# Performance work log

Hardware: AMD Instinct MI355X
Metric: run time of the kernel (lower is better)

Reference implementation:

```python
import jax, jax.numpy as jnp
import numpy as np

B, L, D, NL, VOCAB = 2, 8192, 512, 8, 32
FFT_LEN = 2 * L  # causal linear conv via zero-padded FFT


def layernorm(x, g, b, eps=1e-5):
    mu = jnp.mean(x, axis=-1, keepdims=True)
    var = jnp.var(x, axis=-1, keepdims=True)
    return (x - mu) * jax.lax.rsqrt(var + eps) * g + b


def fftconv(v, h, bias):
    # v: [B, d, L], h: [d, L] long implicit filter, bias: [d] skip (the Hyena 'D' term)
    vf = jnp.fft.rfft(v, n=FFT_LEN)
    hf = jnp.fft.rfft(h, n=FFT_LEN)
    y = jnp.fft.irfft(vf * hf[None], n=FFT_LEN)[..., :L]
    return y + v * bias[:, None]


def short_conv(p, w, b):
    # causal depthwise conv, kernel size 3: p [B, C, L], w [C, 3], b [C]
    pp = jnp.pad(p, ((0, 0), (0, 0), (2, 0)))
    out = jax.lax.conv_general_dilated(pp, w[:, None, :], (1,), 'VALID',
                                       feature_group_count=p.shape[1])
    return out + b[None, :, None]


def setup_inputs() -> dict:
    key = jax.random.key(0)
    ks = jax.random.split(key, 12)
    rn = lambda k, sh, s: jax.random.normal(k, sh, jnp.float32) * s
    d = D
    return {
        'input_ids': jax.random.randint(ks[0], (B, L), 0, VOCAB),
        'emb': rn(ks[1], (VOCAB, d), 0.02),
        'ln1_g': jnp.ones((NL, d)), 'ln1_b': jnp.zeros((NL, d)),
        'Win': rn(ks[2], (NL, d, 3 * d), d ** -0.5), 'bin_': jnp.zeros((NL, 3 * d)),
        'convw': rn(ks[3], (NL, 3 * d, 3), 3 ** -0.5), 'convb': jnp.zeros((NL, 3 * d)),
        'h': rn(ks[4], (NL, d, L), L ** -0.5),  # implicit long filter, materialized
        'Db': rn(ks[5], (NL, d), 1.0),
        'Wout': rn(ks[6], (NL, d, d), d ** -0.5), 'bout': jnp.zeros((NL, d)),
        'ln2_g': jnp.ones((NL, d)), 'ln2_b': jnp.zeros((NL, d)),
        'W1': rn(ks[7], (NL, d, 4 * d), d ** -0.5), 'b1': jnp.zeros((NL, 4 * d)),
        'W2': rn(ks[8], (NL, 4 * d, d), (4 * d) ** -0.5), 'b2': jnp.zeros((NL, d)),
        'lnf_g': jnp.ones((d,)), 'lnf_b': jnp.zeros((d,)),
    }


def reference(input_ids, emb, ln1_g, ln1_b, Win, bin_, convw, convb, h, Db,
              Wout, bout, ln2_g, ln2_b, W1, b1, W2, b2, lnf_g, lnf_b):
    u = emb[input_ids]  # [B, L, d]
    for l in range(NL):  # structural loop over layers
        z = layernorm(u, ln1_g[l], ln1_b[l])
        p = (jnp.einsum('bld,de->ble', z, Win[l]) + bin_[l]).transpose(0, 2, 1)  # [B,3d,L]
        p = short_conv(p, convw[l], convb[l])
        x2, x1, v = jnp.split(p, 3, axis=1)  # each [B, d, L]
        v = fftconv(v * x1, h[l], Db[l])     # gate then FFT long conv (order-2 Hyena)
        y = (v * x2).transpose(0, 2, 1)      # output gate -> [B, L, d]
        u = u + jnp.einsum('bld,de->ble', y, Wout[l]) + bout[l]
        z = layernorm(u, ln2_g[l], ln2_b[l])
        hmid = jax.nn.gelu(jnp.einsum('bld,df->blf', z, W1[l]) + b1[l])
        u = u + jnp.einsum('blf,fd->bld', hmid, W2[l]) + b2[l]
    return layernorm(u, lnf_g, lnf_b)  # last_hidden_state [B, L, d]
```

## Files before the change

### kernel.cpp

```cpp
#include <hip/hip_runtime.h>
#include <hip/hip_bf16.h>
#include <math.h>

#define BB 2
#define LL 8192
#define DD 512
#define NLAYER 8
#define TD 1536
#define HD 2048
#define NFFT 16384
#define BLD (BB*LL*DD)
#define BLH ((size_t)BB*LL*HD)

typedef unsigned short u16;
typedef unsigned int   u32;
typedef __bf16 bf16x8 __attribute__((ext_vector_type(8)));
typedef float  f32x4  __attribute__((ext_vector_type(4)));

__device__ __forceinline__ u16 f2bf(float f) {
    union { float f; u32 u; } v; v.f = f;
    u32 r = v.u + 0x7FFF + ((v.u >> 16) & 1);
    return (u16)(r >> 16);
}
__device__ __forceinline__ float bf2f(u16 h) {
    union { u32 u; float f; } v; v.u = (u32)h << 16; return v.f;
}

__device__ __forceinline__ void async_g2l_16(const u16* g, u16* l) {
    __builtin_amdgcn_global_load_lds(
        (const __attribute__((address_space(1))) void*)g,
        (__attribute__((address_space(3))) void*)l,
        16, 0, 0);
}

__device__ __forceinline__ float2 cmul(float2 a, float2 b) {
    return make_float2(a.x * b.x - a.y * b.y, a.x * b.y + a.y * b.x);
}
__device__ __forceinline__ float2 cmulc(float2 a, float2 b) {
    return make_float2(a.x * b.x + a.y * b.y, a.y * b.x - a.x * b.y);
}
__device__ __forceinline__ float2 cadd(float2 a, float2 b) {
    return make_float2(a.x + b.x, a.y + b.y);
}
__device__ __forceinline__ float2 csub(float2 a, float2 b) {
    return make_float2(a.x - b.x, a.y - b.y);
}
__device__ __forceinline__ int drev14(int x) {
    return ((x & 3) << 12) | (((x >> 2) & 3) << 10) | (((x >> 4) & 3) << 8) |
           (((x >> 6) & 3) << 6) | (((x >> 8) & 3) << 4) | (((x >> 10) & 3) << 2) |
           ((x >> 12) & 3);
}

__global__ void twiddle_kernel(float* twf) {
    int k = blockIdx.x * 256 + threadIdx.x;
    if (k < NFFT) {
        double ang = -2.0 * M_PI * (double)k / (double)NFFT;
        twf[2 * k]     = (float)cos(ang);
        twf[2 * k + 1] = (float)sin(ang);
    }
}

__global__ void embed_kernel(const int* __restrict__ ids,
                             const float* __restrict__ emb,
                             float* __restrict__ u) {
    int i = blockIdx.x * 256 + threadIdx.x;
    if (i < BLD) {
        int row = i >> 9;
        int d   = i & (DD - 1);
        u[i] = emb[ids[row] * DD + d];
    }
}

__global__ __launch_bounds__(256)
void wprep_kernel(const float* __restrict__ W, u16* __restrict__ WtH,
                  u16* __restrict__ WtL, int K, int N, long srcStride, long dstStride) {
    __shared__ float t[64][65];
    const float* src = W + (size_t)blockIdx.z * srcStride;
    u16* dsth = WtH + (size_t)blockIdx.z * dstStride;
    u16* dstl = WtL + (size_t)blockIdx.z * dstStride;
    int n0 = blockIdx.x * 64, k0 = blockIdx.y * 64;
    int tc = threadIdx.x & 63, tr = threadIdx.x >> 6;
    for (int r = tr; r < 64; r += 4)
        t[r][tc] = src[(size_t)(k0 + r) * N + n0 + tc];
    __syncthreads();
    for (int r = tr; r < 64; r += 4) {
        float v = t[tc][r];
        u16 h = f2bf(v);
        dsth[(size_t)(n0 + r) * K + k0 + tc] = h;
        dstl[(size_t)(n0 + r) * K + k0 + tc] = f2bf(v - bf2f(h));
    }
}

template<int MODE>
__global__ __launch_bounds__(128)
void ln_kernel(const float* __restrict__ x, void* __restrict__ out,
               void* __restrict__ outL,
               const float* __restrict__ g, const float* __restrict__ b) {
    int row = blockIdx.x;
    const float4* xr = (const float4*)(x + (size_t)row * DD);
    int t = threadIdx.x;
    float4 v = xr[t];
    float s  = v.x + v.y + v.z + v.w;
    float ss = v.x * v.x + v.y * v.y + v.z * v.z + v.w * v.w;
    for (int off = 32; off; off >>= 1) {
        s  += __shfl_down(s, off);
        ss += __shfl_down(ss, off);
    }
    __shared__ float sm[4];
    if ((t & 63) == 0) { sm[(t >> 6) * 2] = s; sm[(t >> 6) * 2 + 1] = ss; }
    __syncthreads();
    float S = sm[0] + sm[2], SS = sm[1] + sm[3];
    float mu  = S * (1.0f / DD);
    float var = SS * (1.0f / DD) - mu * mu;
    float rs  = rsqrtf(var + 1e-5f);
    float4 gg = ((const float4*)g)[t];
    float4 bb = ((const float4*)b)[t];
    float o[4];
    o[0] = (v.x - mu) * rs * gg.x + bb.x;
    o[1] = (v.y - mu) * rs * gg.y + bb.y;
    o[2] = (v.z - mu) * rs * gg.z + bb.z;
    o[3] = (v.w - mu) * rs * gg.w + bb.w;
    if (MODE == 1) {
        u16 h[4], lo[4];
#pragma unroll
        for (int i = 0; i < 4; i++) {
            h[i]  = f2bf(o[i]);
            lo[i] = f2bf(o[i] - bf2f(h[i]));
        }
        uint2 ph, pl;
        ph.x = (u32)h[0] | ((u32)h[1] << 16);  ph.y = (u32)h[2] | ((u32)h[3] << 16);
        pl.x = (u32)lo[0] | ((u32)lo[1] << 16); pl.y = (u32)lo[2] | ((u32)lo[3] << 16);
        ((uint2*)((u16*)out  + (size_t)row * DD))[t] = ph;
        ((uint2*)((u16*)outL + (size_t)row * DD))[t] = pl;
    } else {
        float4 of = {o[0], o[1], o[2], o[3]};
        ((float4*)((float*)out + (size_t)row * DD))[t] = of;
    }
}

__device__ __forceinline__ float gelu_f(float x) {
    float x3 = x * x * x;
    float t  = tanhf(0.79788456080286541f * (x + 0.044715f * x3));
    return 0.5f * x * (1.0f + t);
}

template<int OUT, bool GELU, int PASSES>
__global__ __launch_bounds__(256)
void mfma_gemm3(const u16* __restrict__ Ah, const u16* __restrict__ Al,
                const u16* __restrict__ Bh, const u16* __restrict__ Bl,
                const float* __restrict__ bias,
                float* __restrict__ Cf, u16* __restrict__ Ch, u16* __restrict__ Cl,
                int M, int N, int K) {
    __shared__ u16 AsH[128 * 32];
    __shared__ u16 AsL[128 * 32];
    __shared__ u16 BsH[128 * 32];
    __shared__ u16 BsL[(PASSES == 3) ? 128 * 32 : 8];
    int m0 = blockIdx.y * 128, n0 = blockIdx.x * 128;
    int tid = threadIdx.x;
    int w = tid >> 6, l = tid & 63;
    int wr = w >> 1, wc = w & 1;

    int ch0 = w * 2, ch1 = ch0 + 1;
    size_t offA0 = (size_t)(m0 + ch0 * 16 + (l >> 2)) * K + (l & 3) * 8;
    size_t offA1 = (size_t)(m0 + ch1 * 16 + (l >> 2)) * K + (l & 3) * 8;
    size_t offB0 = (size_t)(n0 + ch0 * 16 + (l >> 2)) * K + (l & 3) * 8;
    size_t offB1 = (size_t)(n0 + ch1 * 16 + (l >> 2)) * K + (l & 3) * 8;

    f32x4 acc[4][4] = {};
    int arow = wr * 64 + (l & 15);
    int brow = wc * 64 + (l & 15);
    int kc   = (l >> 4) * 8;

    for (int k0 = 0; k0 < K; k0 += 32) {
        async_g2l_16(Ah + offA0 + k0, &AsH[ch0 * 512]);
        async_g2l_16(Ah + offA1 + k0, &AsH[ch1 * 512]);
        async_g2l_16(Al + offA0 + k0, &AsL[ch0 * 512]);
        async_g2l_16(Al + offA1 + k0, &AsL[ch1 * 512]);
        async_g2l_16(Bh + offB0 + k0, &BsH[ch0 * 512]);
        async_g2l_16(Bh + offB1 + k0, &BsH[ch1 * 512]);
        if (PASSES == 3) {
            async_g2l_16(Bl + offB0 + k0, &BsL[ch0 * 512]);
            async_g2l_16(Bl + offB1 + k0, &BsL[ch1 * 512]);
        }
        __syncthreads();
        bf16x8 ah[4], al[4], bh[4], bl[4];
#pragma unroll
        for (int i = 0; i < 4; i++) {
            ah[i] = *(const bf16x8*)&AsH[(arow + i * 16) * 32 + kc];
            al[i] = *(const bf16x8*)&AsL[(arow + i * 16) * 32 + kc];
            bh[i] = *(const bf16x8*)&BsH[(brow + i * 16) * 32 + kc];
            if (PASSES == 3)
                bl[i] = *(const bf16x8*)&BsL[(brow + i * 16) * 32 + kc];
        }
#pragma unroll
        for (int mi = 0; mi < 4; mi++)
#pragma unroll
            for (int ni = 0; ni < 4; ni++) {
                acc[mi][ni] = __builtin_amdgcn_mfma_f32_16x16x32_bf16(
                    ah[mi], bh[ni], acc[mi][ni], 0, 0, 0);
                acc[mi][ni] = __builtin_amdgcn_mfma_f32_16x16x32_bf16(
                    al[mi], bh[ni], acc[mi][ni], 0, 0, 0);
                if (PASSES == 3)
                    acc[mi][ni] = __builtin_amdgcn_mfma_f32_16x16x32_bf16(
                        ah[mi], bl[ni], acc[mi][ni], 0, 0, 0);
            }
        __syncthreads();
    }

    int lr = l >> 4, lc = l & 15;
#pragma unroll
    for (int mi = 0; mi < 4; mi++) {
#pragma unroll
        for (int ni = 0; ni < 4; ni++) {
            int col = n0 + wc * 64 + ni * 16 + lc;
            float bv = bias[col];
            int rowb = m0 + wr * 64 + mi * 16 + lr * 4;
#pragma unroll
            for (int r = 0; r < 4; r++) {
                float v = acc[mi][ni][r] + bv;
                if (GELU) v = gelu_f(v);
                size_t off = (size_t)(rowb + r) * N + col;
                if (OUT == 0) {
                    Cf[off] = v;
                } else if (OUT == 1) {
                    u16 h = f2bf(v);
                    Ch[off] = h;
                    Cl[off] = f2bf(v - bf2f(h));
                } else {
                    Cf[off] += v;
                }
            }
        }
    }
}

__global__ __launch_bounds__(256)
void conv_gate_kernel(const float* __restrict__ p, const float* __restrict__ cw,
                      const float* __restrict__ cb, float* __restrict__ vg,
                      float* __restrict__ x2s) {
    __shared__ float tvg[64][65];
    __shared__ float tx2[64][65];
    int b = blockIdx.z, c0 = blockIdx.y * 64, l0 = blockIdx.x * 64;
    int tc = threadIdx.x & 63, tr = threadIdx.x >> 6;
    const float* pb = p + (size_t)b * LL * TD;
    int cx2 = c0 + tc;
    int cx1 = DD + c0 + tc;
    int cv  = 2 * DD + c0 + tc;
    float w20 = cw[cx2 * 3], w21 = cw[cx2 * 3 + 1], w22 = cw[cx2 * 3 + 2], bx2 = cb[cx2];
    float w10 = cw[cx1 * 3], w11 = cw[cx1 * 3 + 1], w12 = cw[cx1 * 3 + 2], bx1 = cb[cx1];
    float wv0 = cw[cv * 3],  wv1 = cw[cv * 3 + 1],  wv2 = cw[cv * 3 + 2],  bv  = cb[cv];
    for (int r = tr; r < 64; r += 4) {
        int l = l0 + r;
        size_t o0 = (size_t)l * TD;
        float p2a = (l >= 2) ? pb[o0 - 2 * TD + cx2] : 0.f;
        float p1a = (l >= 1) ? pb[o0 - TD + cx2] : 0.f;
        float p0a = pb[o0 + cx2];
        float p2b = (l >= 2) ? pb[o0 - 2 * TD + cx1] : 0.f;
        float p1b = (l >= 1) ? pb[o0 - TD + cx1] : 0.f;
        float p0b = pb[o0 + cx1];
        float p2c = (l >= 2) ? pb[o0 - 2 * TD + cv] : 0.f;
        float p1c = (l >= 1) ? pb[o0 - TD + cv] : 0.f;
        float p0c = pb[o0 + cv];
        float x2v = w20 * p2a + w21 * p1a + w22 * p0a + bx2;
        float x1v = w10 * p2b + w11 * p1b + w12 * p0b + bx1;
        float vv  = wv0 * p2c + wv1 * p1c + wv2 * p0c + bv;
        tx2[r][tc] = x2v;
        tvg[r][tc] = vv * x1v;
    }
    __syncthreads();
    for (int r = tr; r < 64; r += 4) {
        size_t o = ((size_t)b * DD + c0 + r) * LL + l0 + tc;
        vg[o]  = tvg[tc][r];
        x2s[o] = tx2[tc][r];
    }
}

__global__ __launch_bounds__(256)
void ytr_kernel(const float* __restrict__ yg, u16* __restrict__ yh,
                u16* __restrict__ yl) {
    __shared__ float t[64][65];
    int b = blockIdx.z, c0 = blockIdx.y * 64, l0 = blockIdx.x * 64;
    int tc = threadIdx.x & 63, tr = threadIdx.x >> 6;
    for (int r = tr; r < 64; r += 4)
        t[r][tc] = yg[((size_t)b * DD + c0 + r) * LL + l0 + tc];
    __syncthreads();
    for (int r = tr; r < 64; r += 4) {
        float v = t[tc][r];
        u16 h = f2bf(v);
        size_t o = ((size_t)(b * LL + l0 + r)) * DD + c0 + tc;
        yh[o] = h;
        yl[o] = f2bf(v - bf2f(h));
    }
}

__device__ __forceinline__ void fft4_fwd(float2* ld, const float2* __restrict__ tw, int tid) {
    for (int s = 0; s < 7; s++) {
        int lm = 14 - 2 * s, lq = lm - 2;
        int Q = 1 << lq;
        __syncthreads();
        for (int g = tid; g < NFFT / 4; g += 1024) {
            int j = g & (Q - 1);
            int base = ((g >> lq) << lm) + j;
            float2 x0 = ld[base], x1 = ld[base + Q], x2 = ld[base + 2 * Q], x3 = ld[base + 3 * Q];
            float2 a = cadd(x0, x2), b = csub(x0, x2);
            float2 c = cadd(x1, x3), d = csub(x1, x3);
            float2 mid = make_float2(d.y, -d.x);
            float2 u0 = cadd(a, c);
            float2 u1 = cadd(b, mid);
            float2 u2 = csub(a, c);
            float2 u3 = csub(b, mid);
            int e = j << (2 * s);
            if (e) {
                u1 = cmul(u1, tw[e]);
                u2 = cmul(u2, tw[2 * e]);
                u3 = cmul(u3, tw[3 * e]);
            }
            ld[base] = u0; ld[base + Q] = u1; ld[base + 2 * Q] = u2; ld[base + 3 * Q] = u3;
        }
    }
    __syncthreads();
}

__device__ __forceinline__ void fft4_inv(float2* ld, const float2* __restrict__ tw, int tid) {
    for (int s = 6; s >= 0; s--) {
        int lm = 14 - 2 * s, lq = lm - 2;
        int Q = 1 << lq;
        __syncthreads();
        for (int g = tid; g < NFFT / 4; g += 1024) {
            int j = g & (Q - 1);
            int base = ((g >> lq) << lm) + j;
            int e = j << (2 * s);
            float2 v0 = ld[base];
            float2 v1 = ld[base + Q], v2 = ld[base + 2 * Q], v3 = ld[base + 3 * Q];
            if (e) {
                v1 = cmulc(v1, tw[e]);
                v2 = cmulc(v2, tw[2 * e]);
                v3 = cmulc(v3, tw[3 * e]);
            }
            float2 a = cadd(v0, v2), b = csub(v0, v2);
            float2 c = cadd(v1, v3), d = csub(v1, v3);
            float2 id = make_float2(-d.y, d.x);
            ld[base]         = cadd(a, c);
            ld[base + Q]     = cadd(b, id);
            ld[base + 2 * Q] = csub(a, c);
            ld[base + 3 * Q] = csub(b, id);
        }
    }
    __syncthreads();
}


__global__ __launch_bounds__(1024)
void hf_kernel(const float* __restrict__ h, float2* __restrict__ Hf1,
               float2* __restrict__ Hf2, const float* __restrict__ twf) {
    __shared__ float2 ld[NFFT];
    int cp = blockIdx.x;
    const float* h1 = h + (size_t)(2 * cp) * LL;
    const float* h2 = h + (size_t)(2 * cp + 1) * LL;
    const float2* tw = (const float2*)twf;
    int tid = threadIdx.x;
    for (int i = tid; i < LL; i += 1024) ld[i] = make_float2(h1[i], h2[i]);
    for (int i = LL + tid; i < NFFT; i += 1024) ld[i] = make_float2(0.f, 0.f);
    fft4_fwd(ld, tw, tid);
    float2* o1 = Hf1 + (size_t)cp * NFFT;
    float2* o2 = Hf2 + (size_t)cp * NFFT;
    for (int i = tid; i < NFFT / 2; i += 1024) {
        int p  = ((i >> 1) << 2) | (i & 1);
        int k  = drev14(p);
        int kc = (NFFT - k) & (NFFT - 1);
        int pc = drev14(kc);
        float2 Zk = ld[p], Zc = ld[pc];
        float2 F1 = make_float2(0.5f * (Zk.x + Zc.x), 0.5f * (Zk.y - Zc.y));
        float2 F2 = make_float2(0.5f * (Zk.y + Zc.y), 0.5f * (Zc.x - Zk.x));
        o1[p]  = F1;
        o2[p]  = F2;
        o1[pc] = make_float2(F1.x, -F1.y);
        o2[pc] = make_float2(F2.x, -F2.y);
    }
    if (tid == 0) {
        float2 Zk = ld[2];
        o1[2] = make_float2(Zk.x, 0.f);
        o2[2] = make_float2(Zk.y, 0.f);
    }
}

__global__ __launch_bounds__(1024)
void fftconv_kernel(const float* __restrict__ vg, const float* __restrict__ x2s,
                    const float2* __restrict__ Hf1, const float2* __restrict__ Hf2,
                    const float* __restrict__ Db, const float* __restrict__ twf,
                    float* __restrict__ yg) {
    __shared__ float2 ld[NFFT];
    int bcp = blockIdx.x;
    int b = bcp >> 8, cp = bcp & 255;
    int c1 = 2 * cp, c2 = 2 * cp + 1;
    const float* v1 = vg + ((size_t)b * DD + c1) * LL;
    const float* v2 = vg + ((size_t)b * DD + c2) * LL;
    const float2* tw = (const float2*)twf;
    int tid = threadIdx.x;
    for (int i = tid; i < LL; i += 1024) ld[i] = make_float2(v1[i], v2[i]);
    for (int i = LL + tid; i < NFFT; i += 1024) ld[i] = make_float2(0.f, 0.f);
    fft4_fwd(ld, tw, tid);
    const float2* H1 = Hf1 + (size_t)cp * NFFT;
    const float2* H2 = Hf2 + (size_t)cp * NFFT;
    for (int i = tid; i < NFFT / 2; i += 1024) {
        int p  = ((i >> 1) << 2) | (i & 1);
        int k  = drev14(p);
        int kc = (NFFT - k) & (NFFT - 1);
        int pc = drev14(kc);
        float2 Zk = ld[p], Zc = ld[pc];
        float2 F1 = make_float2(0.5f * (Zk.x + Zc.x), 0.5f * (Zk.y - Zc.y));
        float2 F2 = make_float2(0.5f * (Zk.y + Zc.y), 0.5f * (Zc.x - Zk.x));
        float2 c1v = cmul(F1, H1[p]);
        float2 c2v = cmul(F2, H2[p]);
        ld[p]  = make_float2(c1v.x - c2v.y, c1v.y + c2v.x);
        ld[pc] = make_float2(c1v.x + c2v.y, c2v.x - c1v.y);
    }
    if (tid == 0) {
        float2 Zk = ld[2];
        float2 c1v = cmul(make_float2(Zk.x, 0.f), H1[2]);
        float2 c2v = cmul(make_float2(Zk.y, 0.f), H2[2]);
        ld[2] = make_float2(c1v.x - c2v.y, c1v.y + c2v.x);
    }
    fft4_inv(ld, tw, tid);
    float db1 = Db[c1], db2 = Db[c2];
    const float* x21 = x2s + ((size_t)b * DD + c1) * LL;
    const float* x22 = x2s + ((size_t)b * DD + c2) * LL;
    float* o1 = yg + ((size_t)b * DD + c1) * LL;
    float* o2 = yg + ((size_t)b * DD + c2) * LL;
    for (int i = tid; i < LL; i += 1024) {
        float y1 = ld[i].x * (1.0f / NFFT) + v1[i] * db1;
        float y2 = ld[i].y * (1.0f / NFFT) + v2[i] * db2;
        o1[i] = y1 * x21[i];
        o2[i] = y2 * x22[i];
    }
}

extern "C" void kernel_launch(void* const* d_in, const int* in_sizes, int n_in,
                              void* d_out, int out_size, void* d_ws, size_t ws_size,
                              hipStream_t stream) {
    const int*   ids   = (const int*)  d_in[0];
    const float* emb   = (const float*)d_in[1];
    const float* ln1_g = (const float*)d_in[2];
    const float* ln1_b = (const float*)d_in[3];
    const float* Win   = (const float*)d_in[4];
    const float* bin_  = (const float*)d_in[5];
    const float* convw = (const float*)d_in[6];
    const float* convb = (const float*)d_in[7];
    const float* hflt  = (const float*)d_in[8];
    const float* Db    = (const float*)d_in[9];
    const float* Wout  = (const float*)d_in[10];
    const float* bout  = (const float*)d_in[11];
    const float* ln2_g = (const float*)d_in[12];
    const float* ln2_b = (const float*)d_in[13];
    const float* W1    = (const float*)d_in[14];
    const float* b1    = (const float*)d_in[15];
    const float* W2    = (const float*)d_in[16];
    const float* b2    = (const float*)d_in[17];
    const float* lnf_g = (const float*)d_in[18];
    const float* lnf_b = (const float*)d_in[19];

    char* p_ = (char*)d_ws;
    auto alloc = [&](size_t bytes) {
        char* r = p_; p_ += (bytes + 255) & ~(size_t)255; return r;
    };
    float* u   = (float*)alloc((size_t)BLD * 4);
    u16* zh    = (u16*)  alloc((size_t)BLD * 2);
    u16* zl    = (u16*)  alloc((size_t)BLD * 2);
    char* uni  = alloc(2 * BLH * 2);
    float* pf  = (float*)uni;
    float* yg  = (float*)uni;
    u16* hmh   = (u16*)uni;
    u16* hml   = hmh + BLH;
    float* vg  = (float*)alloc((size_t)BLD * 4);
    float* x2s = (float*)alloc((size_t)BLD * 4);
    u16* yh    = (u16*)  alloc((size_t)BLD * 2);
    u16* yl    = (u16*)  alloc((size_t)BLD * 2);
    float2* Hf1 = (float2*)alloc((size_t)(DD / 2) * NFFT * 8);
    float2* Hf2 = (float2*)alloc((size_t)(DD / 2) * NFFT * 8);
    float* tw  = (float*)alloc((size_t)2 * NFFT * 4);
    u16* WtInH = (u16*)alloc((size_t)NLAYER * TD * DD * 2);
    u16* WtInL = (u16*)alloc((size_t)NLAYER * TD * DD * 2);
    u16* WtOutH= (u16*)alloc((size_t)NLAYER * DD * DD * 2);
    u16* WtOutL= (u16*)alloc((size_t)NLAYER * DD * DD * 2);
    u16* Wt1H  = (u16*)alloc((size_t)NLAYER * DD * HD * 2);
    u16* Wt1L  = (u16*)alloc((size_t)NLAYER * DD * HD * 2);
    u16* Wt2H  = (u16*)alloc((size_t)NLAYER * HD * DD * 2);
    u16* Wt2L  = (u16*)alloc((size_t)NLAYER * HD * DD * 2);

    twiddle_kernel<<<(NFFT + 255) / 256, 256, 0, stream>>>(tw);
    embed_kernel<<<(BLD + 255) / 256, 256, 0, stream>>>(ids, emb, u);
    wprep_kernel<<<dim3(TD / 64, DD / 64, NLAYER), 256, 0, stream>>>(
        Win, WtInH, WtInL, DD, TD, (long)DD * TD, (long)TD * DD);
    wprep_kernel<<<dim3(DD / 64, DD / 64, NLAYER), 256, 0, stream>>>(
        Wout, WtOutH, WtOutL, DD, DD, (long)DD * DD, (long)DD * DD);
    wprep_kernel<<<dim3(HD / 64, DD / 64, NLAYER), 256, 0, stream>>>(
        W1, Wt1H, Wt1L, DD, HD, (long)DD * HD, (long)DD * HD);
    wprep_kernel<<<dim3(DD / 64, HD / 64, NLAYER), 256, 0, stream>>>(
        W2, Wt2H, Wt2L, HD, DD, (long)HD * DD, (long)HD * DD);

    for (int l = 0; l < NLAYER; l++) {
        ln_kernel<1><<<BB * LL, 128, 0, stream>>>(u, zh, zl,
            ln1_g + l * DD, ln1_b + l * DD);

        mfma_gemm3<0, false, 3><<<dim3(TD / 128, (BB * LL) / 128), 256, 0, stream>>>(
            zh, zl, WtInH + (size_t)l * TD * DD, WtInL + (size_t)l * TD * DD,
            bin_ + (size_t)l * TD, pf, nullptr, nullptr, BB * LL, TD, DD);

        conv_gate_kernel<<<dim3(LL / 64, DD / 64, BB), 256, 0, stream>>>(
            pf, convw + (size_t)l * TD * 3, convb + (size_t)l * TD, vg, x2s);

        hf_kernel<<<DD / 2, 1024, 0, stream>>>(hflt + (size_t)l * DD * LL, Hf1, Hf2, tw);

        fftconv_kernel<<<BB * (DD / 2), 1024, 0, stream>>>(
            vg, x2s, Hf1, Hf2, Db + (size_t)l * DD, tw, yg);

        ytr_kernel<<<dim3(LL / 64, DD / 64, BB), 256, 0, stream>>>(yg, yh, yl);

        mfma_gemm3<2, false, 3><<<dim3(DD / 128, (BB * LL) / 128), 256, 0, stream>>>(
            yh, yl, WtOutH + (size_t)l * DD * DD, WtOutL + (size_t)l * DD * DD,
            bout + (size_t)l * DD, u, nullptr, nullptr, BB * LL, DD, DD);

        ln_kernel<1><<<BB * LL, 128, 0, stream>>>(u, zh, zl,
            ln2_g + l * DD, ln2_b + l * DD);

        mfma_gemm3<1, true, 2><<<dim3(HD / 128, (BB * LL) / 128), 256, 0, stream>>>(
            zh, zl, Wt1H + (size_t)l * DD * HD, Wt1L + (size_t)l * DD * HD,
            b1 + (size_t)l * HD, nullptr, hmh, hml, BB * LL, HD, DD);

        mfma_gemm3<2, false, 2><<<dim3(DD / 128, (BB * LL) / 128), 256, 0, stream>>>(
            hmh, hml, Wt2H + (size_t)l * HD * DD, Wt2L + (size_t)l * HD * DD,
            b2 + (size_t)l * DD, u, nullptr, nullptr, BB * LL, DD, HD);
    }

    ln_kernel<0><<<BB * LL, 128, 0, stream>>>(u, (float*)d_out, nullptr, lnf_g, lnf_b);
}
```

Before: 5.501 ms.

## Replace paired-channel 16K complex FFT with per-channel 8K half-length real FFT

```diff
diff --git a/kernel.cpp b/kernel.cpp
--- a/kernel.cpp
+++ b/kernel.cpp
@@ -9,6 +9,7 @@
 #define TD 1536
 #define HD 2048
 #define NFFT 16384
+#define NHALF 8192
 #define BLD (BB*LL*DD)
 #define BLH ((size_t)BB*LL*HD)
 
@@ -45,10 +46,12 @@
 __device__ __forceinline__ float2 csub(float2 a, float2 b) {
     return make_float2(a.x - b.x, a.y - b.y);
 }
-__device__ __forceinline__ int drev14(int x) {
-    return ((x & 3) << 12) | (((x >> 2) & 3) << 10) | (((x >> 4) & 3) << 8) |
-           (((x >> 6) & 3) << 6) | (((x >> 8) & 3) << 4) | (((x >> 10) & 3) << 2) |
-           ((x >> 12) & 3);
+__device__ __forceinline__ int drev12(int m) {
+    return ((m & 3) << 10) | (((m >> 2) & 3) << 8) | (((m >> 4) & 3) << 6) |
+           (((m >> 6) & 3) << 4) | (((m >> 8) & 3) << 2) | ((m >> 10) & 3);
+}
+__device__ __forceinline__ int perm8k(int k) {
+    return ((k & 1) << 12) + drev12(k >> 1);
 }
 
 __global__ void twiddle_kernel(float* twf) {
@@ -293,14 +296,22 @@
     }
 }
 
-__device__ __forceinline__ void fft4_fwd(float2* ld, const float2* __restrict__ tw, int tid) {
-    for (int s = 0; s < 7; s++) {
-        int lm = 14 - 2 * s, lq = lm - 2;
+__device__ __forceinline__ void fft8192_fwd(float2* ld, const float2* __restrict__ tw, int tid) {
+    __syncthreads();
+    for (int n = tid; n < 4096; n += 1024) {
+        float2 a = ld[n], b = ld[n + 4096];
+        ld[n] = cadd(a, b);
+        float2 d = csub(a, b);
+        ld[n + 4096] = n ? cmul(d, tw[2 * n]) : d;
+    }
+    for (int s = 0; s < 6; s++) {
+        int lm = 12 - 2 * s, lq = lm - 2;
         int Q = 1 << lq;
         __syncthreads();
-        for (int g = tid; g < NFFT / 4; g += 1024) {
-            int j = g & (Q - 1);
-            int base = ((g >> lq) << lm) + j;
+        for (int g = tid; g < 2048; g += 1024) {
+            int half = g >> 10, gg = g & 1023;
+            int j = gg & (Q - 1);
+            int base = (half << 12) + ((gg >> lq) << lm) + j;
             float2 x0 = ld[base], x1 = ld[base + Q], x2 = ld[base + 2 * Q], x3 = ld[base + 3 * Q];
             float2 a = cadd(x0, x2), b = csub(x0, x2);
             float2 c = cadd(x1, x3), d = csub(x1, x3);
@@ -311,9 +322,9 @@
             float2 u3 = csub(b, mid);
             int e = j << (2 * s);
             if (e) {
-                u1 = cmul(u1, tw[e]);
-                u2 = cmul(u2, tw[2 * e]);
-                u3 = cmul(u3, tw[3 * e]);
+                u1 = cmul(u1, tw[4 * e]);
+                u2 = cmul(u2, tw[8 * e]);
+                u3 = cmul(u3, tw[12 * e]);
             }
             ld[base] = u0; ld[base + Q] = u1; ld[base + 2 * Q] = u2; ld[base + 3 * Q] = u3;
         }
@@ -321,21 +332,22 @@
     __syncthreads();
 }
 
-__device__ __forceinline__ void fft4_inv(float2* ld, const float2* __restrict__ tw, int tid) {
-    for (int s = 6; s >= 0; s--) {
-        int lm = 14 - 2 * s, lq = lm - 2;
+__device__ __forceinline__ void fft8192_inv(float2* ld, const float2* __restrict__ tw, int tid) {
+    for (int s = 5; s >= 0; s--) {
+        int lm = 12 - 2 * s, lq = lm - 2;
         int Q = 1 << lq;
         __syncthreads();
-        for (int g = tid; g < NFFT / 4; g += 1024) {
-            int j = g & (Q - 1);
-            int base = ((g >> lq) << lm) + j;
+        for (int g = tid; g < 2048; g += 1024) {
+            int half = g >> 10, gg = g & 1023;
+            int j = gg & (Q - 1);
+            int base = (half << 12) + ((gg >> lq) << lm) + j;
             int e = j << (2 * s);
             float2 v0 = ld[base];
             float2 v1 = ld[base + Q], v2 = ld[base + 2 * Q], v3 = ld[base + 3 * Q];
             if (e) {
-                v1 = cmulc(v1, tw[e]);
-                v2 = cmulc(v2, tw[2 * e]);
-                v3 = cmulc(v3, tw[3 * e]);
+                v1 = cmulc(v1, tw[4 * e]);
+                v2 = cmulc(v2, tw[8 * e]);
+                v3 = cmulc(v3, tw[12 * e]);
             }
             float2 a = cadd(v0, v2), b = csub(v0, v2);
             float2 c = cadd(v1, v3), d = csub(v1, v3);
@@ -347,91 +359,101 @@
         }
     }
     __syncthreads();
-}
-
-
-__global__ __launch_bounds__(1024)
-void hf_kernel(const float* __restrict__ h, float2* __restrict__ Hf1,
-               float2* __restrict__ Hf2, const float* __restrict__ twf) {
-    __shared__ float2 ld[NFFT];
-    int cp = blockIdx.x;
-    const float* h1 = h + (size_t)(2 * cp) * LL;
-    const float* h2 = h + (size_t)(2 * cp + 1) * LL;
+    for (int n = tid; n < 4096; n += 1024) {
+        float2 a = ld[n];
+        float2 b = ld[n + 4096];
+        if (n) b = cmulc(b, tw[2 * n]);
+        ld[n] = cadd(a, b);
+        ld[n + 4096] = csub(a, b);
+    }
+    __syncthreads();
+}
+
+__global__ __launch_bounds__(1024, 8)
+void hf_kernel(const float* __restrict__ h, float2* __restrict__ HfA,
+               float2* __restrict__ HfB, const float* __restrict__ twf) {
+    __shared__ float2 ld[NHALF];
+    int c = blockIdx.x;
+    const float2* hp = (const float2*)(h + (size_t)c * LL);
     const float2* tw = (const float2*)twf;
     int tid = threadIdx.x;
-    for (int i = tid; i < LL; i += 1024) ld[i] = make_float2(h1[i], h2[i]);
-    for (int i = LL + tid; i < NFFT; i += 1024) ld[i] = make_float2(0.f, 0.f);
-    fft4_fwd(ld, tw, tid);
-    float2* o1 = Hf1 + (size_t)cp * NFFT;
-    float2* o2 = Hf2 + (size_t)cp * NFFT;
-    for (int i = tid; i < NFFT / 2; i += 1024) {
-        int p  = ((i >> 1) << 2) | (i & 1);
-        int k  = drev14(p);
-        int kc = (NFFT - k) & (NFFT - 1);
-        int pc = drev14(kc);
-        float2 Zk = ld[p], Zc = ld[pc];
-        float2 F1 = make_float2(0.5f * (Zk.x + Zc.x), 0.5f * (Zk.y - Zc.y));
-        float2 F2 = make_float2(0.5f * (Zk.y + Zc.y), 0.5f * (Zc.x - Zk.x));
-        o1[p]  = F1;
-        o2[p]  = F2;
-        o1[pc] = make_float2(F1.x, -F1.y);
-        o2[pc] = make_float2(F2.x, -F2.y);
-    }
-    if (tid == 0) {
-        float2 Zk = ld[2];
-        o1[2] = make_float2(Zk.x, 0.f);
-        o2[2] = make_float2(Zk.y, 0.f);
-    }
-}
-
-__global__ __launch_bounds__(1024)
+    for (int n = tid; n < 4096; n += 1024) ld[n] = hp[n];
+    for (int n = 4096 + tid; n < NHALF; n += 1024) ld[n] = make_float2(0.f, 0.f);
+    fft8192_fwd(ld, tw, tid);
+    float2* oa = HfA + (size_t)c * NHALF;
+    float2* ob = HfB + (size_t)c * NHALF;
+    for (int k = tid; k <= 4096; k += 1024) {
+        int kc = (NHALF - k) & (NHALF - 1);
+        int p = perm8k(k), pc = perm8k(kc);
+        float2 A = ld[p], B = ld[pc];
+        float2 E = make_float2(0.5f * (A.x + B.x), 0.5f * (A.y - B.y));
+        float2 O = make_float2(0.5f * (A.y + B.y), -0.5f * (A.x - B.x));
+        float2 t = tw[k];
+        float2 tO = cmul(t, O);
+        float2 X1 = cadd(E, tO);
+        float2 X2 = csub(E, tO);
+        oa[k] = X1;
+        ob[k] = X2;
+        if (kc != k) {
+            oa[kc] = make_float2(X2.x, -X2.y);
+            ob[kc] = make_float2(X1.x, -X1.y);
+        }
+    }
+}
+
+__global__ __launch_bounds__(1024, 8)
 void fftconv_kernel(const float* __restrict__ vg, const float* __restrict__ x2s,
-                    const float2* __restrict__ Hf1, const float2* __restrict__ Hf2,
+                    const float2* __restrict__ HfA, const float2* __restrict__ HfB,
                     const float* __restrict__ Db, const float* __restrict__ twf,
                     float* __restrict__ yg) {
-    __shared__ float2 ld[NFFT];
-    int bcp = blockIdx.x;
-    int b = bcp >> 8, cp = bcp & 255;
-    int c1 = 2 * cp, c2 = 2 * cp + 1;
-    const float* v1 = vg + ((size_t)b * DD + c1) * LL;
-    const float* v2 = vg + ((size_t)b * DD + c2) * LL;
+    __shared__ float2 ld[NHALF];
+    int bc = blockIdx.x;
+    int c  = bc & (DD - 1);
+    const float2* vp  = (const float2*)(vg  + (size_t)bc * LL);
+    const float2* x2p = (const float2*)(x2s + (size_t)bc * LL);
+    float2*       op  = (float2*)(yg + (size_t)bc * LL);
     const float2* tw = (const float2*)twf;
     int tid = threadIdx.x;
-    for (int i = tid; i < LL; i += 1024) ld[i] = make_float2(v1[i], v2[i]);
-    for (int i = LL + tid; i < NFFT; i += 1024) ld[i] = make_float2(0.f, 0.f);
-    fft4_fwd(ld, tw, tid);
-    const float2* H1 = Hf1 + (size_t)cp * NFFT;
-    const float2* H2 = Hf2 + (size_t)cp * NFFT;
-    for (int i = tid; i < NFFT / 2; i += 1024) {
-        int p  = ((i >> 1) << 2) | (i & 1);
-        int k  = drev14(p);
-        int kc = (NFFT - k) & (NFFT - 1);
-        int pc = drev14(kc);
-        float2 Zk = ld[p], Zc = ld[pc];
-        float2 F1 = make_float2(0.5f * (Zk.x + Zc.x), 0.5f * (Zk.y - Zc.y));
-        float2 F2 = make_float2(0.5f * (Zk.y + Zc.y), 0.5f * (Zc.x - Zk.x));
-        float2 c1v = cmul(F1, H1[p]);
-        float2 c2v = cmul(F2, H2[p]);
-        ld[p]  = make_float2(c1v.x - c2v.y, c1v.y + c2v.x);
-        ld[pc] = make_float2(c1v.x + c2v.y, c2v.x - c1v.y);
-    }
-    if (tid == 0) {
-        float2 Zk = ld[2];
-        float2 c1v = cmul(make_float2(Zk.x, 0.f), H1[2]);
-        float2 c2v = cmul(make_float2(Zk.y, 0.f), H2[2]);
-        ld[2] = make_float2(c1v.x - c2v.y, c1v.y + c2v.x);
-    }
-    fft4_inv(ld, tw, tid);
-    float db1 = Db[c1], db2 = Db[c2];
-    const float* x21 = x2s + ((size_t)b * DD + c1) * LL;
-    const float* x22 = x2s + ((size_t)b * DD + c2) * LL;
-    float* o1 = yg + ((size_t)b * DD + c1) * LL;
-    float* o2 = yg + ((size_t)b * DD + c2) * LL;
-    for (int i = tid; i < LL; i += 1024) {
-        float y1 = ld[i].x * (1.0f / NFFT) + v1[i] * db1;
-        float y2 = ld[i].y * (1.0f / NFFT) + v2[i] * db2;
-        o1[i] = y1 * x21[i];
-        o2[i] = y2 * x22[i];
+    for (int n = tid; n < 4096; n += 1024) ld[n] = vp[n];
+    for (int n = 4096 + tid; n < NHALF; n += 1024) ld[n] = make_float2(0.f, 0.f);
+    fft8192_fwd(ld, tw, tid);
+    const float2* Ha = HfA + (size_t)c * NHALF;
+    const float2* Hb = HfB + (size_t)c * NHALF;
+    for (int k = tid; k <= 4096; k += 1024) {
+        int kc = (NHALF - k) & (NHALF - 1);
+        int p = perm8k(k), pc = perm8k(kc);
+        float2 A = ld[p], B = ld[pc];
+        float2 E = make_float2(0.5f * (A.x + B.x), 0.5f * (A.y - B.y));
+        float2 O = make_float2(0.5f * (A.y + B.y), -0.5f * (A.x - B.x));
+        float2 t = tw[k];
+        float2 tO = cmul(t, O);
+        float2 X1 = cadd(E, tO);
+        float2 X2 = csub(E, tO);
+        float2 Y1 = cmul(X1, Ha[k]);
+        float2 Y2 = cmul(X2, Hb[k]);
+        float2 S  = make_float2(0.5f * (Y1.x + Y2.x), 0.5f * (Y1.y + Y2.y));
+        float2 Dd = make_float2(0.5f * (Y1.x - Y2.x), 0.5f * (Y1.y - Y2.y));
+        ld[p] = cadd(S, cmul(make_float2(t.y, t.x), Dd));
+        if (kc != k) {
+            float2 X1c = make_float2(X2.x, -X2.y);
+            float2 X2c = make_float2(X1.x, -X1.y);
+            float2 Y1c = cmul(X1c, Ha[kc]);
+            float2 Y2c = cmul(X2c, Hb[kc]);
+            float2 Sc = make_float2(0.5f * (Y1c.x + Y2c.x), 0.5f * (Y1c.y + Y2c.y));
+            float2 Dc = make_float2(0.5f * (Y1c.x - Y2c.x), 0.5f * (Y1c.y - Y2c.y));
+            ld[pc] = cadd(Sc, cmul(make_float2(t.y, -t.x), Dc));
+        }
+    }
+    fft8192_inv(ld, tw, tid);
+    float db = Db[c];
+    const float inv = 1.0f / (float)NHALF;
+    for (int n = tid; n < 4096; n += 1024) {
+        float2 w  = ld[n];
+        float2 vv = vp[n];
+        float2 xx = x2p[n];
+        float y0 = w.x * inv + vv.x * db;
+        float y1 = w.y * inv + vv.y * db;
+        op[n] = make_float2(y0 * xx.x, y1 * xx.y);
     }
 }
 
@@ -475,8 +497,8 @@
     float* x2s = (float*)alloc((size_t)BLD * 4);
     u16* yh    = (u16*)  alloc((size_t)BLD * 2);
     u16* yl    = (u16*)  alloc((size_t)BLD * 2);
-    float2* Hf1 = (float2*)alloc((size_t)(DD / 2) * NFFT * 8);
-    float2* Hf2 = (float2*)alloc((size_t)(DD / 2) * NFFT * 8);
+    float2* HfA = (float2*)alloc((size_t)DD * NHALF * 8);
+    float2* HfB = (float2*)alloc((size_t)DD * NHALF * 8);
     float* tw  = (float*)alloc((size_t)2 * NFFT * 4);
     u16* WtInH = (u16*)alloc((size_t)NLAYER * TD * DD * 2);
     u16* WtInL = (u16*)alloc((size_t)NLAYER * TD * DD * 2);
@@ -509,14 +531,14 @@
         conv_gate_kernel<<<dim3(LL / 64, DD / 64, BB), 256, 0, stream>>>(
             pf, convw + (size_t)l * TD * 3, convb + (size_t)l * TD, vg, x2s);
 
-        hf_kernel<<<DD / 2, 1024, 0, stream>>>(hflt + (size_t)l * DD * LL, Hf1, Hf2, tw);
-
-        fftconv_kernel<<<BB * (DD / 2), 1024, 0, stream>>>(
-            vg, x2s, Hf1, Hf2, Db + (size_t)l * DD, tw, yg);
+        hf_kernel<<<DD, 1024, 0, stream>>>(hflt + (size_t)l * DD * LL, HfA, HfB, tw);
+
+        fftconv_kernel<<<BB * DD, 1024, 0, stream>>>(
+            vg, x2s, HfA, HfB, Db + (size_t)l * DD, tw, yg);
 
         ytr_kernel<<<dim3(LL / 64, DD / 64, BB), 256, 0, stream>>>(yg, yh, yl);
 
-        mfma_gemm3<2, false, 3><<<dim3(DD / 128, (BB * LL) / 128), 256, 0, stream>>>(
+        mfma_gemm3<2, false, 2><<<dim3(DD / 128, (BB * LL) / 128), 256, 0, stream>>>(
             yh, yl, WtOutH + (size_t)l * DD * DD, WtOutL + (size_t)l * DD * DD,
             bout + (size_t)l * DD, u, nullptr, nullptr, BB * LL, DD, DD);
 
```

Result: faster. 5.376 ms (-2.3%).
